# Kernel optimization log

Measured on AMD Instinct MI355X. Metric: run time of the kernel, lower is better.

## Reference

```python
import jax, jax.numpy as jnp
import numpy as np

B, C, N = 4, 256, 4096
C4 = C // 4  # q/k projection dim (channels // 4)
BN_EPS = 1e-5


def setup_inputs() -> dict:
    key = jax.random.key(0)
    ks = jax.random.split(key, 4)
    s = 0.05
    return {
        "x": jax.random.normal(ks[0], (B, C, N), jnp.float32),
        # q_conv and k_conv share this weight in the original module
        "wq": jax.random.normal(ks[1], (C4, C), jnp.float32) * s,
        "wv": jax.random.normal(ks[2], (C, C), jnp.float32) * s,
        "bv": jnp.zeros((C,), jnp.float32),
        "wt": jax.random.normal(ks[3], (C, C), jnp.float32) * s,
        "bt": jnp.zeros((C,), jnp.float32),
        "gamma": jnp.ones((C,), jnp.float32),
        "beta": jnp.zeros((C,), jnp.float32),
        "running_mean": jnp.zeros((C,), jnp.float32),
        "running_var": jnp.ones((C,), jnp.float32),
    }


def reference(x, wq, wv, bv, wt, bt, gamma, beta, running_mean, running_var):
    # 1x1 Conv1d == channel matmul. q/k share wq.
    q = jnp.einsum('oc,bcn->bno', wq, x)            # [B, N, C4]
    k = jnp.einsum('oc,bcn->bon', wq, x)            # [B, C4, N]
    energy = jnp.einsum('bno,bom->bnm', q, k)       # [B, N, N]
    attn = jax.nn.softmax(energy, axis=-1)
    # offset-attention L1 re-normalization over dim 1 (query axis)
    attn = attn / (1e-9 + attn.sum(axis=1, keepdims=True))
    v = jnp.einsum('oc,bcn->bon', wv, x) + bv[None, :, None]   # [B, C, N]
    # x_r[b,c,n] = sum_m v[b,c,m] * attn[b,n,m]
    x_r = jnp.einsum('bcm,bnm->bcn', v, attn)       # [B, C, N]
    t = jnp.einsum('oc,bcn->bon', wt, x - x_r) + bt[None, :, None]
    # BatchNorm1d in inference mode (running stats)
    inv = jax.lax.rsqrt(running_var + BN_EPS)
    bn = (t - running_mean[None, :, None]) * (gamma * inv)[None, :, None] + beta[None, :, None]
    return x + jax.nn.relu(bn)
```

## Files before the change

kernel.cpp:

```cpp
#include <hip/hip_runtime.h>
#include <math.h>

namespace {

constexpr int B_ = 4;
constexpr int C_ = 256;
constexpr int C4_ = 64;
constexpr int N_ = 4096;

typedef __attribute__((ext_vector_type(8))) short bf16x8;
typedef __attribute__((ext_vector_type(4))) float f32x4;
typedef __attribute__((ext_vector_type(16))) float f32x16;

__device__ __forceinline__ unsigned short bf16_rne(float f) {
    unsigned u = __float_as_uint(f);
    u += 0x7fffu + ((u >> 16) & 1u);
    return (unsigned short)(u >> 16);
}

__device__ __forceinline__ void g2l16(const unsigned short* g, unsigned short* l) {
    __builtin_amdgcn_global_load_lds(
        (const __attribute__((address_space(1))) unsigned int*)g,
        (__attribute__((address_space(3))) unsigned int*)l, 16, 0, 0);
}

__global__ __launch_bounds__(256) void cvt_kernel(
        const float* __restrict__ wq, const float* __restrict__ wv,
        const float* __restrict__ wt, unsigned short* __restrict__ wfrag,
        unsigned short* __restrict__ wtb) {
    const int i = (blockIdx.x * 256 + threadIdx.x) * 4;
    const float* src;
    unsigned short* dst;
    if (i < 81920) {
        src = (i < 16384) ? (wq + i) : (wv + (i - 16384));
        const int o = i >> 8, c = i & 255;
        const int gro = o >> 4, l15 = o & 15;
        const int ch = c >> 5, quad = (c >> 3) & 3, e = c & 7;
        dst = wfrag + (((gro * 8 + ch) * 64 + quad * 16 + l15) * 8 + e);
    } else {
        src = wt + (i - 81920);
        dst = wtb + (i - 81920);
    }
    const float4 f = *reinterpret_cast<const float4*>(src);
    ushort4 u;
    u.x = bf16_rne(f.x); u.y = bf16_rne(f.y);
    u.z = bf16_rne(f.z); u.w = bf16_rne(f.w);
    *reinterpret_cast<ushort4*>(dst) = u;
}

__global__ __launch_bounds__(1024, 4) void proj_kernel(
        const float* __restrict__ x, const unsigned short* __restrict__ wfragb,
        const float* __restrict__ bv, unsigned short* __restrict__ qkT,
        unsigned short* __restrict__ v) {
    __shared__ unsigned short xs[2][64][42];
    const int b = blockIdx.y;
    const int n0 = blockIdx.x * 64;
    const int tid = threadIdx.x;
    const int wave = tid >> 6, lane = tid & 63;
    const int ws = wave & 3, oq = wave >> 2;
    const int quad = lane >> 4, l15 = lane & 15;
    const int ca = tid >> 6, na = tid & 63;
    const int cb = (tid + 1024) >> 6, nb2 = (tid + 1024) & 63;
    f32x4 acc[5];
#pragma unroll
    for (int ot = 0; ot < 5; ++ot) acc[ot] = (f32x4){0.f, 0.f, 0.f, 0.f};
    xs[0][na][ca] = bf16_rne(x[((size_t)b * C_ + ca) * N_ + n0 + na]);
    xs[0][nb2][cb] = bf16_rne(x[((size_t)b * C_ + cb) * N_ + n0 + nb2]);
    __syncthreads();
    for (int ch = 0; ch < 8; ++ch) {
        const int buf = ch & 1;
        float la = 0.f, lb = 0.f;
        if (ch < 7) {
            la = x[((size_t)b * C_ + (ch + 1) * 32 + ca) * N_ + n0 + na];
            lb = x[((size_t)b * C_ + (ch + 1) * 32 + cb) * N_ + n0 + nb2];
        }
        const bf16x8 a = *reinterpret_cast<const bf16x8*>(&xs[buf][ws * 16 + l15][quad * 8]);
#pragma unroll
        for (int ot = 0; ot < 5; ++ot) {
            const int gro = oq * 5 + ot;
            const bf16x8 wb = *reinterpret_cast<const bf16x8*>(
                wfragb + (size_t)(((gro * 8 + ch) * 64 + lane) * 8));
            acc[ot] = __builtin_amdgcn_mfma_f32_16x16x32_bf16(a, wb, acc[ot], 0, 0, 0);
        }
        if (ch < 7) {
            xs[buf ^ 1][na][ca] = bf16_rne(la);
            xs[buf ^ 1][nb2][cb] = bf16_rne(lb);
        }
        __syncthreads();
    }
    const int n = n0 + ws * 16 + quad * 4;
#pragma unroll
    for (int ot = 0; ot < 5; ++ot) {
        const int gro = oq * 5 + ot;
        if (gro < 4) {
            const int o = gro * 16 + l15;
#pragma unroll
            for (int r = 0; r < 4; ++r)
                qkT[((size_t)b * N_ + n + r) * C4_ + o] = bf16_rne(acc[ot][r]);
        } else {
            const int c = (gro - 4) * 16 + l15;
            const float bb = bv[c];
            ushort4 u;
            u.x = bf16_rne(acc[ot][0] + bb);
            u.y = bf16_rne(acc[ot][1] + bb);
            u.z = bf16_rne(acc[ot][2] + bb);
            u.w = bf16_rne(acc[ot][3] + bb);
            *reinterpret_cast<ushort4*>(&v[((size_t)b * C_ + c) * N_ + n]) = u;
        }
    }
}

__global__ __launch_bounds__(1024, 4) void rowsum_kernel(
        const unsigned short* __restrict__ qkT, float* __restrict__ rowsuminv) {
    __shared__ unsigned short kt[3][256][64];
    __shared__ float red[2][8][2][16];
    const int gid = blockIdx.x;
    const int xcd = gid & 7;
    const int b = xcd >> 1;
    const int n0 = ((((unsigned)gid >> 3) << 1) | (xcd & 1)) * 64;
    const int tid = threadIdx.x;
    const int wave = tid >> 6, lane = tid & 63;
    const int nt = wave >> 3, ms = wave & 7;
    const int l31 = lane & 31, h = lane >> 5;
    const unsigned short* qb = qkT + (size_t)b * N_ * C4_;
    const int rowA = lane >> 3;
    const int swc = ((lane & 7) ^ rowA) * 8;
    const int w16 = wave * 16;
    const int r7 = l31 & 7;
    const unsigned short* qrow = qb + (size_t)(n0 + nt * 32 + l31) * C4_ + h * 8;
    bf16x8 qa[4];
#pragma unroll
    for (int j = 0; j < 4; ++j)
        qa[j] = *reinterpret_cast<const bf16x8*>(qrow + j * 16);
    asm volatile("s_waitcnt vmcnt(0)" ::: "memory");
#define RS_STAGE(sidx, bufS)                                                  \
    do {                                                                      \
        g2l16(qb + (size_t)((sidx) * 256 + w16 + rowA) * C4_ + swc,           \
              &kt[bufS][w16][0]);                                             \
        g2l16(qb + (size_t)((sidx) * 256 + w16 + 8 + rowA) * C4_ + swc,       \
              &kt[bufS][w16 + 8][0]);                                         \
    } while (0)
    RS_STAGE(0, 0);
    RS_STAGE(1, 1);
    asm volatile("s_waitcnt vmcnt(2)" ::: "memory");
    __builtin_amdgcn_s_barrier();
    f32x16 acc = (f32x16){0.f, 0.f, 0.f, 0.f, 0.f, 0.f, 0.f, 0.f,
                          0.f, 0.f, 0.f, 0.f, 0.f, 0.f, 0.f, 0.f};
    int bufR = 0;
#pragma unroll 1
    for (int t = 0; t < 16; ++t) {
        if (t <= 13) {
            int bufS = bufR + 2; if (bufS >= 3) bufS -= 3;
            RS_STAGE(t + 2, bufS);
        }
        f32x16 z = (f32x16){0.f, 0.f, 0.f, 0.f, 0.f, 0.f, 0.f, 0.f,
                            0.f, 0.f, 0.f, 0.f, 0.f, 0.f, 0.f, 0.f};
        __builtin_amdgcn_s_setprio(1);
#pragma unroll
        for (int j = 0; j < 4; ++j) {
            const bf16x8 kb = *reinterpret_cast<const bf16x8*>(
                &kt[bufR][ms * 32 + l31][(j * 16 + h * 8) ^ (r7 << 3)]);
            z = __builtin_amdgcn_mfma_f32_32x32x16_bf16(qa[j], kb, z, 0, 0, 0);
        }
        __builtin_amdgcn_s_setprio(0);
#pragma unroll
        for (int r = 0; r < 16; ++r) acc[r] += __expf(z[r]);
        asm volatile("s_waitcnt lgkmcnt(0)" ::: "memory");
        if (t <= 13)      asm volatile("s_waitcnt vmcnt(2)" ::: "memory");
        else if (t == 14) asm volatile("s_waitcnt vmcnt(0)" ::: "memory");
        __builtin_amdgcn_s_barrier();
        ++bufR; if (bufR >= 3) bufR = 0;
    }
#undef RS_STAGE
#pragma unroll
    for (int r = 0; r < 16; ++r) {
        float s = acc[r];
#pragma unroll
        for (int k = 1; k <= 16; k <<= 1) s += __shfl_xor(s, k, 64);
        if (l31 == 0) red[nt][ms][h][r] = s;
    }
    __syncthreads();
    if (tid < 64) {
        const int v = tid & 31, nt2 = tid >> 5;
        const int reg = (v & 3) | ((v >> 3) << 2);
        const int hh = (v >> 2) & 1;
        float sum = 0.f;
#pragma unroll
        for (int m = 0; m < 8; ++m) sum += red[nt2][m][hh][reg];
        rowsuminv[(size_t)b * N_ + n0 + nt2 * 32 + v] = 1.0f / sum;
    }
}

__global__ __launch_bounds__(1024, 4) void colsum_kernel(
        const unsigned short* __restrict__ qkT, const float* __restrict__ rowsuminv,
        float* __restrict__ colsuminv) {
    __shared__ float rl[N_];
    __shared__ unsigned short qt[3][256][64];
    __shared__ float red2[8][2][32];
    const int gid = blockIdx.x;
    const int xcd = gid & 7;
    const int b = xcd >> 1;
    const int m0 = ((((unsigned)gid >> 3) << 1) | (xcd & 1)) * 64;
    const int tid = threadIdx.x;
    const int wave = tid >> 6, lane = tid & 63;
    const int ms2 = wave >> 3, ns = wave & 7;
    const int l31 = lane & 31, h = lane >> 5;
    const unsigned short* qb = qkT + (size_t)b * N_ * C4_;
    const int rowA = lane >> 3;
    const int swc = ((lane & 7) ^ rowA) * 8;
    const int w16 = wave * 16;
    const int r7 = l31 & 7;
    for (int i = tid; i < N_; i += 1024) rl[i] = rowsuminv[(size_t)b * N_ + i];
    const unsigned short* krow = qb + (size_t)(m0 + ms2 * 32 + l31) * C4_ + h * 8;
    bf16x8 kbf[4];
#pragma unroll
    for (int j = 0; j < 4; ++j)
        kbf[j] = *reinterpret_cast<const bf16x8*>(krow + j * 16);
    asm volatile("s_waitcnt vmcnt(0)" ::: "memory");
#define CS_STAGE(sidx, bufS)                                                  \
    do {                                                                      \
        g2l16(qb + (size_t)((sidx) * 256 + w16 + rowA) * C4_ + swc,           \
              &qt[bufS][w16][0]);                                             \
        g2l16(qb + (size_t)((sidx) * 256 + w16 + 8 + rowA) * C4_ + swc,       \
              &qt[bufS][w16 + 8][0]);                                         \
    } while (0)
    CS_STAGE(0, 0);
    CS_STAGE(1, 1);
    asm volatile("s_waitcnt vmcnt(2)" ::: "memory");
    asm volatile("s_waitcnt lgkmcnt(0)" ::: "memory");
    __builtin_amdgcn_s_barrier();
    float csa = 0.f;
    int bufR = 0;
#pragma unroll 1
    for (int t = 0; t < 16; ++t) {
        if (t <= 13) {
            int bufS = bufR + 2; if (bufS >= 3) bufS -= 3;
            CS_STAGE(t + 2, bufS);
        }
        f32x16 z = (f32x16){0.f, 0.f, 0.f, 0.f, 0.f, 0.f, 0.f, 0.f,
                            0.f, 0.f, 0.f, 0.f, 0.f, 0.f, 0.f, 0.f};
        __builtin_amdgcn_s_setprio(1);
#pragma unroll
        for (int j = 0; j < 4; ++j) {
            const bf16x8 qa = *reinterpret_cast<const bf16x8*>(
                &qt[bufR][ns * 32 + l31][(j * 16 + h * 8) ^ (r7 << 3)]);
            z = __builtin_amdgcn_mfma_f32_32x32x16_bf16(qa, kbf[j], z, 0, 0, 0);
        }
        __builtin_amdgcn_s_setprio(0);
        const int nb = t * 256 + ns * 32 + 4 * h;
#pragma unroll
        for (int r = 0; r < 16; ++r)
            csa += __expf(z[r]) * rl[nb + (r & 3) + 8 * (r >> 2)];
        asm volatile("s_waitcnt lgkmcnt(0)" ::: "memory");
        if (t <= 13)      asm volatile("s_waitcnt vmcnt(2)" ::: "memory");
        else if (t == 14) asm volatile("s_waitcnt vmcnt(0)" ::: "memory");
        __builtin_amdgcn_s_barrier();
        ++bufR; if (bufR >= 3) bufR = 0;
    }
#undef CS_STAGE
    csa += __shfl_xor(csa, 32, 64);
    if (h == 0) red2[ns][ms2][l31] = csa;
    __syncthreads();
    if (tid < 64) {
        const int ml = tid & 31, mg = tid >> 5;
        float sum = 0.f;
#pragma unroll
        for (int n = 0; n < 8; ++n) sum += red2[n][mg][ml];
        colsuminv[(size_t)b * N_ + m0 + mg * 32 + ml] = 1.0f / (1e-9f + sum);
    }
}

__global__ __launch_bounds__(1024, 4) void final_kernel(
        const float* __restrict__ x, const unsigned short* __restrict__ qkT,
        const unsigned short* __restrict__ v, const unsigned short* __restrict__ wtb,
        const float* __restrict__ rowsuminv, const float* __restrict__ colsuminv,
        const float* __restrict__ bt, const float* __restrict__ gamma,
        const float* __restrict__ beta, const float* __restrict__ rmean,
        const float* __restrict__ rvar, float* __restrict__ out) {
    __shared__ union {
        struct {
            unsigned short vt[3][256][64];
            unsigned short kt[3][64][64];
        } s;
        unsigned short dsm[64][268];
    } u;
    __shared__ unsigned short p_sh[2][4][16][68];
    __shared__ float ci[N_];
    const int gid = blockIdx.x;
    const int xcd = gid & 7;
    const int b = xcd >> 1;
    const int n0 = ((((unsigned)gid >> 3) << 1) | (xcd & 1)) * 64;
    const int tid = threadIdx.x;
    const int wave = tid >> 6, lane = tid & 63;
    const int ws = wave & 3, g = wave >> 2;
    const int quad = lane >> 4, l15 = lane & 15;
    const unsigned short* qb = qkT + (size_t)b * N_ * C4_;
    const unsigned short* vbg = v + (size_t)b * C_ * N_;
    const int rowA = lane >> 3;
    const int swc = ((lane & 7) ^ rowA) * 8;
    const int w8 = wave * 8;
    const int r7 = l15 & 7;
    const int c0s = (quad * 8) ^ (r7 << 3);
    const int c1s = (32 + quad * 8) ^ (r7 << 3);
    const unsigned short* qrow = qb + (size_t)(n0 + ws * 16 + l15) * C4_;
    const bf16x8 q0 = *reinterpret_cast<const bf16x8*>(qrow + quad * 8);
    const bf16x8 q1 = *reinterpret_cast<const bf16x8*>(qrow + 32 + quad * 8);
    const float rli = rowsuminv[(size_t)b * N_ + n0 + ws * 16 + l15];
    {
        const float4 c4 = *reinterpret_cast<const float4*>(colsuminv + (size_t)b * N_ + tid * 4);
        *reinterpret_cast<float4*>(&ci[tid * 4]) = c4;
    }
    asm volatile("s_waitcnt vmcnt(0)" ::: "memory");
#define STAGE_VT(sidx, bufS)                                                            \
    do {                                                                                \
        g2l16(vbg + (size_t)(w8 + rowA) * N_ + (sidx) * 64 + swc,                       \
              &u.s.vt[bufS][w8][0]);                                                    \
        g2l16(vbg + (size_t)(w8 + 128 + rowA) * N_ + (sidx) * 64 + swc,                 \
              &u.s.vt[bufS][w8 + 128][0]);                                              \
    } while (0)
#define STAGE_KT(sidx, bufS)                                                            \
    do {                                                                                \
        if (wave < 8)                                                                   \
            g2l16(qb + (size_t)((sidx) * 64 + w8 + rowA) * C4_ + swc,                   \
                  &u.s.kt[bufS][w8][0]);                                                \
    } while (0)
    STAGE_VT(0, 0);
    STAGE_KT(0, 0);
    STAGE_KT(1, 1);
    asm volatile("s_waitcnt vmcnt(0)" ::: "memory");
    asm volatile("s_waitcnt lgkmcnt(0)" ::: "memory");
    __builtin_amdgcn_s_barrier();
    f32x4 acc[4];
#pragma unroll
    for (int j = 0; j < 4; ++j) acc[j] = (f32x4){0.f, 0.f, 0.f, 0.f};
    int bR = 0;
#pragma unroll 1
    for (int t = 0; t < 64; ++t) {
        int bN = bR + 1; if (bN >= 3) bN -= 3;
        int bN2 = bR + 2; if (bN2 >= 3) bN2 -= 3;
        if (t <= 62) STAGE_VT(t + 1, bN);
        if (t <= 61) STAGE_KT(t + 2, bN2);
        {
            const unsigned short(*ktb)[64] = u.s.kt[bR];
            const bf16x8 ka0 = *reinterpret_cast<const bf16x8*>(&ktb[g * 16 + l15][c0s]);
            const bf16x8 ka1 = *reinterpret_cast<const bf16x8*>(&ktb[g * 16 + l15][c1s]);
            f32x4 z = {0.f, 0.f, 0.f, 0.f};
            z = __builtin_amdgcn_mfma_f32_16x16x32_bf16(ka0, q0, z, 0, 0, 0);
            z = __builtin_amdgcn_mfma_f32_16x16x32_bf16(ka1, q1, z, 0, 0, 0);
            const float4 civ = *reinterpret_cast<const float4*>(&ci[t * 64 + g * 16 + quad * 4]);
            ushort4 pk;
            pk.x = bf16_rne(__expf(z[0]) * rli * civ.x);
            pk.y = bf16_rne(__expf(z[1]) * rli * civ.y);
            pk.z = bf16_rne(__expf(z[2]) * rli * civ.z);
            pk.w = bf16_rne(__expf(z[3]) * rli * civ.w);
            *reinterpret_cast<ushort4*>(&p_sh[t & 1][ws][l15][g * 16 + quad * 4]) = pk;
        }
        if (t) {
            int bP = bR - 1; if (bP < 0) bP += 3;
            const bf16x8 pa0 = *reinterpret_cast<const bf16x8*>(
                &p_sh[(t - 1) & 1][ws][l15][quad * 8]);
            const bf16x8 pa1 = *reinterpret_cast<const bf16x8*>(
                &p_sh[(t - 1) & 1][ws][l15][32 + quad * 8]);
            const unsigned short(*vtb)[64] = u.s.vt[bP];
            __builtin_amdgcn_s_setprio(1);
#pragma unroll
            for (int j = 0; j < 4; ++j) {
                const int vr = (g * 4 + j) * 16 + l15;
                const bf16x8 vb0 = *reinterpret_cast<const bf16x8*>(&vtb[vr][c0s]);
                const bf16x8 vb1 = *reinterpret_cast<const bf16x8*>(&vtb[vr][c1s]);
                acc[j] = __builtin_amdgcn_mfma_f32_16x16x32_bf16(pa0, vb0, acc[j], 0, 0, 0);
                acc[j] = __builtin_amdgcn_mfma_f32_16x16x32_bf16(pa1, vb1, acc[j], 0, 0, 0);
            }
            __builtin_amdgcn_s_setprio(0);
        }
        asm volatile("s_waitcnt lgkmcnt(0)" ::: "memory");
        if (t <= 61) {
            if (wave < 8) asm volatile("s_waitcnt vmcnt(3)" ::: "memory");
            else          asm volatile("s_waitcnt vmcnt(2)" ::: "memory");
        } else if (t == 62) {
            asm volatile("s_waitcnt vmcnt(2)" ::: "memory");
        } else {
            asm volatile("s_waitcnt vmcnt(0)" ::: "memory");
        }
        __builtin_amdgcn_s_barrier();
        ++bR; if (bR >= 3) bR = 0;
    }
    {
        const bf16x8 pa0 = *reinterpret_cast<const bf16x8*>(&p_sh[1][ws][l15][quad * 8]);
        const bf16x8 pa1 = *reinterpret_cast<const bf16x8*>(&p_sh[1][ws][l15][32 + quad * 8]);
        const unsigned short(*vtb)[64] = u.s.vt[0];
#pragma unroll
        for (int j = 0; j < 4; ++j) {
            const int vr = (g * 4 + j) * 16 + l15;
            const bf16x8 vb0 = *reinterpret_cast<const bf16x8*>(&vtb[vr][c0s]);
            const bf16x8 vb1 = *reinterpret_cast<const bf16x8*>(&vtb[vr][c1s]);
            acc[j] = __builtin_amdgcn_mfma_f32_16x16x32_bf16(pa0, vb0, acc[j], 0, 0, 0);
            acc[j] = __builtin_amdgcn_mfma_f32_16x16x32_bf16(pa1, vb1, acc[j], 0, 0, 0);
        }
    }
    __syncthreads();
#pragma unroll
    for (int j = 0; j < 4; ++j) {
        const int c = (g * 4 + j) * 16 + l15;
        const float4 xv = *reinterpret_cast<const float4*>(
            &x[((size_t)b * C_ + c) * N_ + n0 + ws * 16 + quad * 4]);
        const float xvr[4] = {xv.x, xv.y, xv.z, xv.w};
#pragma unroll
        for (int r = 0; r < 4; ++r)
            u.dsm[ws * 16 + quad * 4 + r][c] = bf16_rne(xvr[r] - acc[j][r]);
    }
    __syncthreads();
    bf16x8 da[8];
#pragma unroll
    for (int k = 0; k < 8; ++k)
        da[k] = *reinterpret_cast<const bf16x8*>(&u.dsm[ws * 16 + l15][k * 32 + quad * 8]);
    f32x4 tacc[4];
#pragma unroll
    for (int j = 0; j < 4; ++j) tacc[j] = (f32x4){0.f, 0.f, 0.f, 0.f};
#pragma unroll
    for (int j = 0; j < 4; ++j) {
        const int ot = g * 4 + j;
#pragma unroll
        for (int k = 0; k < 8; ++k) {
            const bf16x8 wb = *reinterpret_cast<const bf16x8*>(
                wtb + (size_t)(ot * 16 + l15) * C_ + k * 32 + quad * 8);
            tacc[j] = __builtin_amdgcn_mfma_f32_16x16x32_bf16(da[k], wb, tacc[j], 0, 0, 0);
        }
    }
#pragma unroll
    for (int j = 0; j < 4; ++j) {
        const int o = (g * 4 + j) * 16 + l15;
        const float gg = gamma[o] * rsqrtf(rvar[o] + 1e-5f);
        const float mn = rmean[o], bbet = beta[o], bo = bt[o];
        const size_t oi = ((size_t)b * C_ + o) * N_ + n0 + ws * 16 + quad * 4;
        const float4 xo = *reinterpret_cast<const float4*>(&x[oi]);
        float4 res;
        res.x = xo.x + fmaxf((tacc[j][0] + bo - mn) * gg + bbet, 0.f);
        res.y = xo.y + fmaxf((tacc[j][1] + bo - mn) * gg + bbet, 0.f);
        res.z = xo.z + fmaxf((tacc[j][2] + bo - mn) * gg + bbet, 0.f);
        res.w = xo.w + fmaxf((tacc[j][3] + bo - mn) * gg + bbet, 0.f);
        *reinterpret_cast<float4*>(&out[oi]) = res;
    }
#undef STAGE_VT
#undef STAGE_KT
}

}

extern "C" void kernel_launch(void* const* d_in, const int* in_sizes, int n_in,
                              void* d_out, int out_size, void* d_ws, size_t ws_size,
                              hipStream_t stream) {
    const float* x = (const float*)d_in[0];
    const float* wq = (const float*)d_in[1];
    const float* wv = (const float*)d_in[2];
    const float* bv = (const float*)d_in[3];
    const float* wt = (const float*)d_in[4];
    const float* bt = (const float*)d_in[5];
    const float* gamma = (const float*)d_in[6];
    const float* beta = (const float*)d_in[7];
    const float* rmean = (const float*)d_in[8];
    const float* rvar = (const float*)d_in[9];
    float* out = (float*)d_out;

    char* base = (char*)d_ws;
    unsigned short* qkT = (unsigned short*)base;
    unsigned short* vw = (unsigned short*)(base + (2u << 20));
    unsigned short* wtb = (unsigned short*)(base + (10u << 20));
    unsigned short* wfrag = (unsigned short*)(base + (10u << 20) + (128u << 10));
    float* rowsuminv = (float*)(base + (10u << 20) + (288u << 10));
    float* colsuminv = (float*)(base + (10u << 20) + (352u << 10));

    cvt_kernel<<<dim3(144), dim3(256), 0, stream>>>(wq, wv, wt, wfrag, wtb);
    proj_kernel<<<dim3(N_ / 64, B_), dim3(1024), 0, stream>>>(x, wfrag, bv, qkT, vw);
    rowsum_kernel<<<dim3(N_ / 64 * B_), dim3(1024), 0, stream>>>(qkT, rowsuminv);
    colsum_kernel<<<dim3(N_ / 64 * B_), dim3(1024), 0, stream>>>(qkT, rowsuminv, colsuminv);
    final_kernel<<<dim3(N_ / 64 * B_), dim3(1024), 0, stream>>>(
        x, qkT, vw, wtb, rowsuminv, colsuminv, bt, gamma, beta, rmean, rvar, out);
}
```

Baseline: 246.6 us.

## Materialize bf16 attention matrix in colsum pass and reuse it in final matmul

When the workspace is large enough, the column-sum kernel writes the row-normalized exp(energy) tile as bf16 into a global N×N buffer per batch. The final kernel then reads that matrix instead of recomputing QK^T and exp. Column normalization is folded into V by a small scaling kernel. This trades recomputing attention for writing and reading about 128 MB of bf16 probabilities through HBM, and adds a rounding step on V.

Result: faster. 223.0 us (-9.6%).

```diff
diff --git a/kernel.cpp b/kernel.cpp
--- a/kernel.cpp
+++ b/kernel.cpp
@@ -16,6 +16,10 @@
     unsigned u = __float_as_uint(f);
     u += 0x7fffu + ((u >> 16) & 1u);
     return (unsigned short)(u >> 16);
+}
+
+__device__ __forceinline__ float bf16_to_f(unsigned short s) {
+    return __uint_as_float(((unsigned)s) << 16);
 }
 
 __device__ __forceinline__ void g2l16(const unsigned short* g, unsigned short* l) {
@@ -191,11 +195,13 @@
     }
 }
 
+template <int WP>
 __global__ __launch_bounds__(1024, 4) void colsum_kernel(
         const unsigned short* __restrict__ qkT, const float* __restrict__ rowsuminv,
-        float* __restrict__ colsuminv) {
+        float* __restrict__ colsuminv, unsigned short* __restrict__ ptg) {
     __shared__ float rl[N_];
     __shared__ unsigned short qt[3][256][64];
+    __shared__ unsigned short ptile[16][32][40];
     __shared__ float red2[8][2][32];
     const int gid = blockIdx.x;
     const int xcd = gid & 7;
@@ -249,11 +255,30 @@
         __builtin_amdgcn_s_setprio(0);
         const int nb = t * 256 + ns * 32 + 4 * h;
 #pragma unroll
-        for (int r = 0; r < 16; ++r)
-            csa += __expf(z[r]) * rl[nb + (r & 3) + 8 * (r >> 2)];
+        for (int r = 0; r < 16; ++r) {
+            const float ex = __expf(z[r]) * rl[nb + (r & 3) + 8 * (r >> 2)];
+            csa += ex;
+            if constexpr (WP)
+                ptile[wave][(r & 3) + 8 * (r >> 2) + 4 * h][l31] = bf16_rne(ex);
+        }
+        if constexpr (WP) {
+            asm volatile("s_waitcnt lgkmcnt(0)" ::: "memory");
+            const int r2 = lane >> 1, hf = lane & 1;
+            const bf16x8 pr0 = *reinterpret_cast<const bf16x8*>(&ptile[wave][r2][hf * 16]);
+            const bf16x8 pr1 = *reinterpret_cast<const bf16x8*>(&ptile[wave][r2][hf * 16 + 8]);
+            unsigned short* pd = ptg + ((size_t)b * N_ + t * 256 + ns * 32 + r2) * N_
+                                 + m0 + ms2 * 32 + hf * 16;
+            *reinterpret_cast<bf16x8*>(pd) = pr0;
+            *reinterpret_cast<bf16x8*>(pd + 8) = pr1;
+        }
         asm volatile("s_waitcnt lgkmcnt(0)" ::: "memory");
-        if (t <= 13)      asm volatile("s_waitcnt vmcnt(2)" ::: "memory");
-        else if (t == 14) asm volatile("s_waitcnt vmcnt(0)" ::: "memory");
+        if constexpr (WP) {
+            if (t <= 13)      asm volatile("s_waitcnt vmcnt(4)" ::: "memory");
+            else if (t == 14) asm volatile("s_waitcnt vmcnt(2)" ::: "memory");
+        } else {
+            if (t <= 13)      asm volatile("s_waitcnt vmcnt(2)" ::: "memory");
+            else if (t == 14) asm volatile("s_waitcnt vmcnt(0)" ::: "memory");
+        }
         __builtin_amdgcn_s_barrier();
         ++bufR; if (bufR >= 3) bufR = 0;
     }
@@ -267,6 +292,152 @@
 #pragma unroll
         for (int n = 0; n < 8; ++n) sum += red2[n][mg][ml];
         colsuminv[(size_t)b * N_ + m0 + mg * 32 + ml] = 1.0f / (1e-9f + sum);
+    }
+}
+
+__global__ __launch_bounds__(256) void scale_v_kernel(
+        unsigned short* __restrict__ v, const float* __restrict__ colsuminv) {
+    const size_t i8 = ((size_t)blockIdx.x * 256 + threadIdx.x) * 8;
+    const int b = (int)(i8 >> 20);
+    const int m = (int)(i8 & 4095);
+    const float* cv = colsuminv + ((size_t)b << 12) + m;
+    const float4 c0 = *reinterpret_cast<const float4*>(cv);
+    const float4 c1 = *reinterpret_cast<const float4*>(cv + 4);
+    const ushort4 a = *reinterpret_cast<const ushort4*>(v + i8);
+    const ushort4 bb = *reinterpret_cast<const ushort4*>(v + i8 + 4);
+    ushort4 oa, ob;
+    oa.x = bf16_rne(bf16_to_f(a.x) * c0.x); oa.y = bf16_rne(bf16_to_f(a.y) * c0.y);
+    oa.z = bf16_rne(bf16_to_f(a.z) * c0.z); oa.w = bf16_rne(bf16_to_f(a.w) * c0.w);
+    ob.x = bf16_rne(bf16_to_f(bb.x) * c1.x); ob.y = bf16_rne(bf16_to_f(bb.y) * c1.y);
+    ob.z = bf16_rne(bf16_to_f(bb.z) * c1.z); ob.w = bf16_rne(bf16_to_f(bb.w) * c1.w);
+    *reinterpret_cast<ushort4*>(v + i8) = oa;
+    *reinterpret_cast<ushort4*>(v + i8 + 4) = ob;
+}
+
+__global__ __launch_bounds__(1024, 4) void final7_kernel(
+        const float* __restrict__ x, const unsigned short* __restrict__ ptg,
+        const unsigned short* __restrict__ v, const unsigned short* __restrict__ wtb,
+        const float* __restrict__ bt, const float* __restrict__ gamma,
+        const float* __restrict__ beta, const float* __restrict__ rmean,
+        const float* __restrict__ rvar, float* __restrict__ out) {
+    __shared__ union {
+        struct {
+            unsigned short vt[3][256][64];
+            unsigned short pt[3][64][64];
+        } s;
+        unsigned short dsm[64][268];
+    } u;
+    const int gid = blockIdx.x;
+    const int xcd = gid & 7;
+    const int b = xcd >> 1;
+    const int n0 = ((((unsigned)gid >> 3) << 1) | (xcd & 1)) * 64;
+    const int tid = threadIdx.x;
+    const int wave = tid >> 6, lane = tid & 63;
+    const int ws = wave & 3, g = wave >> 2;
+    const int quad = lane >> 4, l15 = lane & 15;
+    const unsigned short* pb = ptg + ((size_t)b * N_ + n0) * N_;
+    const unsigned short* vbg = v + (size_t)b * C_ * N_;
+    const int rowA = lane >> 3;
+    const int swc = ((lane & 7) ^ rowA) * 8;
+    const int w8 = wave * 8;
+    const int r7 = l15 & 7;
+    const int c0s = (quad * 8) ^ (r7 << 3);
+    const int c1s = (32 + quad * 8) ^ (r7 << 3);
+    asm volatile("s_waitcnt vmcnt(0)" ::: "memory");
+#define STAGE7(sidx, bufS)                                                              \
+    do {                                                                                \
+        g2l16(vbg + (size_t)(w8 + rowA) * N_ + (sidx) * 64 + swc,                       \
+              &u.s.vt[bufS][w8][0]);                                                    \
+        g2l16(vbg + (size_t)(w8 + 128 + rowA) * N_ + (sidx) * 64 + swc,                 \
+              &u.s.vt[bufS][w8 + 128][0]);                                              \
+        if (wave < 8)                                                                   \
+            g2l16(pb + (size_t)(w8 + rowA) * N_ + (sidx) * 64 + swc,                    \
+                  &u.s.pt[bufS][w8][0]);                                                \
+    } while (0)
+    STAGE7(0, 0);
+    STAGE7(1, 1);
+    if (wave < 8) asm volatile("s_waitcnt vmcnt(3)" ::: "memory");
+    else          asm volatile("s_waitcnt vmcnt(2)" ::: "memory");
+    __builtin_amdgcn_s_barrier();
+    f32x4 acc[4];
+#pragma unroll
+    for (int j = 0; j < 4; ++j) acc[j] = (f32x4){0.f, 0.f, 0.f, 0.f};
+    int bR = 0;
+#pragma unroll 1
+    for (int t = 0; t < 64; ++t) {
+        if (t <= 61) {
+            int bN2 = bR + 2; if (bN2 >= 3) bN2 -= 3;
+            STAGE7(t + 2, bN2);
+        }
+        {
+            const bf16x8 pa0 = *reinterpret_cast<const bf16x8*>(
+                &u.s.pt[bR][ws * 16 + l15][c0s]);
+            const bf16x8 pa1 = *reinterpret_cast<const bf16x8*>(
+                &u.s.pt[bR][ws * 16 + l15][c1s]);
+            const unsigned short(*vtb)[64] = u.s.vt[bR];
+            __builtin_amdgcn_s_setprio(1);
+#pragma unroll
+            for (int j = 0; j < 4; ++j) {
+                const int vr = (g * 4 + j) * 16 + l15;
+                const bf16x8 vb0 = *reinterpret_cast<const bf16x8*>(&vtb[vr][c0s]);
+                const bf16x8 vb1 = *reinterpret_cast<const bf16x8*>(&vtb[vr][c1s]);
+                acc[j] = __builtin_amdgcn_mfma_f32_16x16x32_bf16(pa0, vb0, acc[j], 0, 0, 0);
+                acc[j] = __builtin_amdgcn_mfma_f32_16x16x32_bf16(pa1, vb1, acc[j], 0, 0, 0);
+            }
+            __builtin_amdgcn_s_setprio(0);
+        }
+        asm volatile("s_waitcnt lgkmcnt(0)" ::: "memory");
+        if (t <= 61) {
+            if (wave < 8) asm volatile("s_waitcnt vmcnt(3)" ::: "memory");
+            else          asm volatile("s_waitcnt vmcnt(2)" ::: "memory");
+        } else if (t == 62) {
+            asm volatile("s_waitcnt vmcnt(0)" ::: "memory");
+        }
+        __builtin_amdgcn_s_barrier();
+        ++bR; if (bR >= 3) bR = 0;
+    }
+#undef STAGE7
+#pragma unroll
+    for (int j = 0; j < 4; ++j) {
+        const int c = (g * 4 + j) * 16 + l15;
+        const float4 xv = *reinterpret_cast<const float4*>(
+            &x[((size_t)b * C_ + c) * N_ + n0 + ws * 16 + quad * 4]);
+        const float xvr[4] = {xv.x, xv.y, xv.z, xv.w};
+#pragma unroll
+        for (int r = 0; r < 4; ++r)
+            u.dsm[ws * 16 + quad * 4 + r][c] = bf16_rne(xvr[r] - acc[j][r]);
+    }
+    __syncthreads();
+    bf16x8 da[8];
+#pragma unroll
+    for (int k = 0; k < 8; ++k)
+        da[k] = *reinterpret_cast<const bf16x8*>(&u.dsm[ws * 16 + l15][k * 32 + quad * 8]);
+    f32x4 tacc[4];
+#pragma unroll
+    for (int j = 0; j < 4; ++j) tacc[j] = (f32x4){0.f, 0.f, 0.f, 0.f};
+#pragma unroll
+    for (int j = 0; j < 4; ++j) {
+        const int ot = g * 4 + j;
+#pragma unroll
+        for (int k = 0; k < 8; ++k) {
+            const bf16x8 wb = *reinterpret_cast<const bf16x8*>(
+                wtb + (size_t)(ot * 16 + l15) * C_ + k * 32 + quad * 8);
+            tacc[j] = __builtin_amdgcn_mfma_f32_16x16x32_bf16(da[k], wb, tacc[j], 0, 0, 0);
+        }
+    }
+#pragma unroll
+    for (int j = 0; j < 4; ++j) {
+        const int o = (g * 4 + j) * 16 + l15;
+        const float gg = gamma[o] * rsqrtf(rvar[o] + 1e-5f);
+        const float mn = rmean[o], bbet = beta[o], bo = bt[o];
+        const size_t oi = ((size_t)b * C_ + o) * N_ + n0 + ws * 16 + quad * 4;
+        const float4 xo = *reinterpret_cast<const float4*>(&x[oi]);
+        float4 res;
+        res.x = xo.x + fmaxf((tacc[j][0] + bo - mn) * gg + bbet, 0.f);
+        res.y = xo.y + fmaxf((tacc[j][1] + bo - mn) * gg + bbet, 0.f);
+        res.z = xo.z + fmaxf((tacc[j][2] + bo - mn) * gg + bbet, 0.f);
+        res.w = xo.w + fmaxf((tacc[j][3] + bo - mn) * gg + bbet, 0.f);
+        *reinterpret_cast<float4*>(&out[oi]) = res;
     }
 }
 
@@ -469,11 +640,22 @@
     unsigned short* wfrag = (unsigned short*)(base + (10u << 20) + (128u << 10));
     float* rowsuminv = (float*)(base + (10u << 20) + (288u << 10));
     float* colsuminv = (float*)(base + (10u << 20) + (352u << 10));
+    unsigned short* ptg = (unsigned short*)(base + (16ull << 20));
+    const bool big = ws_size >= (144ull << 20);
 
     cvt_kernel<<<dim3(144), dim3(256), 0, stream>>>(wq, wv, wt, wfrag, wtb);
     proj_kernel<<<dim3(N_ / 64, B_), dim3(1024), 0, stream>>>(x, wfrag, bv, qkT, vw);
     rowsum_kernel<<<dim3(N_ / 64 * B_), dim3(1024), 0, stream>>>(qkT, rowsuminv);
-    colsum_kernel<<<dim3(N_ / 64 * B_), dim3(1024), 0, stream>>>(qkT, rowsuminv, colsuminv);
-    final_kernel<<<dim3(N_ / 64 * B_), dim3(1024), 0, stream>>>(
-        x, qkT, vw, wtb, rowsuminv, colsuminv, bt, gamma, beta, rmean, rvar, out);
-}
+    if (big) {
+        colsum_kernel<1><<<dim3(N_ / 64 * B_), dim3(1024), 0, stream>>>(
+            qkT, rowsuminv, colsuminv, ptg);
+        scale_v_kernel<<<dim3(2048), dim3(256), 0, stream>>>(vw, colsuminv);
+        final7_kernel<<<dim3(N_ / 64 * B_), dim3(1024), 0, stream>>>(
+            x, ptg, vw, wtb, bt, gamma, beta, rmean, rvar, out);
+    } else {
+        colsum_kernel<0><<<dim3(N_ / 64 * B_), dim3(1024), 0, stream>>>(
+            qkT, rowsuminv, colsuminv, nullptr);
+        final_kernel<<<dim3(N_ / 64 * B_), dim3(1024), 0, stream>>>(
+            x, qkT, vw, wtb, rowsuminv, colsuminv, bt, gamma, beta, rmean, rvar, out);
+    }
+}
```

## Materialize exp(QK^T) once in bf16 and reuse it for colsum and final

Applied to the files above, without the earlier changes.

The rowsum kernel now writes the full exp(energy) matrix in bf16 to global workspace, about 128 MB. It also computes weighted partial column sums, which replaces the separate colsum kernel that recomputed QK^T and exp. The column normalisation is folded into V through a new scale kernel, and the row normalisation is applied in the epilogue of the final kernel. The final kernel streams the stored P tiles instead of recomputing them with MFMA and exp. This trades recomputation for a very large HBM write and read of the attention matrix, and adds two small kernels.

After: 226.0 us. 1.09x faster.

```diff
diff --git a/kernel.cpp b/kernel.cpp
--- a/kernel.cpp
+++ b/kernel.cpp
@@ -16,6 +16,10 @@
     unsigned u = __float_as_uint(f);
     u += 0x7fffu + ((u >> 16) & 1u);
     return (unsigned short)(u >> 16);
+}
+
+__device__ __forceinline__ float bf16_to_f(unsigned short s) {
+    return __uint_as_float(((unsigned)s) << 16);
 }
 
 __device__ __forceinline__ void g2l16(const unsigned short* g, unsigned short* l) {
@@ -111,9 +115,12 @@
 }
 
 __global__ __launch_bounds__(1024, 4) void rowsum_kernel(
-        const unsigned short* __restrict__ qkT, float* __restrict__ rowsuminv) {
+        const unsigned short* __restrict__ qkT, float* __restrict__ rowsuminv,
+        unsigned short* __restrict__ etg, float* __restrict__ psum) {
     __shared__ unsigned short kt[3][256][64];
+    __shared__ unsigned short etile[16][32][40];
     __shared__ float red[2][8][2][16];
+    __shared__ float rls[64];
     const int gid = blockIdx.x;
     const int xcd = gid & 7;
     const int b = xcd >> 1;
@@ -164,14 +171,29 @@
         }
         __builtin_amdgcn_s_setprio(0);
 #pragma unroll
-        for (int r = 0; r < 16; ++r) acc[r] += __expf(z[r]);
+        for (int r = 0; r < 16; ++r) {
+            const float ex = __expf(z[r]);
+            acc[r] += ex;
+            etile[wave][(r & 3) + 8 * (r >> 2) + 4 * h][l31] = bf16_rne(ex);
+        }
         asm volatile("s_waitcnt lgkmcnt(0)" ::: "memory");
-        if (t <= 13)      asm volatile("s_waitcnt vmcnt(2)" ::: "memory");
-        else if (t == 14) asm volatile("s_waitcnt vmcnt(0)" ::: "memory");
+        {
+            const int r2 = lane >> 1, hf = lane & 1;
+            const bf16x8 pr0 = *reinterpret_cast<const bf16x8*>(&etile[wave][r2][hf * 16]);
+            const bf16x8 pr1 = *reinterpret_cast<const bf16x8*>(&etile[wave][r2][hf * 16 + 8]);
+            unsigned short* pd = etg + ((size_t)b * N_ + n0 + nt * 32 + r2) * N_
+                                 + t * 256 + ms * 32 + hf * 16;
+            *reinterpret_cast<bf16x8*>(pd) = pr0;
+            *reinterpret_cast<bf16x8*>(pd + 8) = pr1;
+        }
+        asm volatile("s_waitcnt lgkmcnt(0)" ::: "memory");
+        if (t <= 13)      asm volatile("s_waitcnt vmcnt(4)" ::: "memory");
+        else if (t == 14) asm volatile("s_waitcnt vmcnt(2)" ::: "memory");
         __builtin_amdgcn_s_barrier();
         ++bufR; if (bufR >= 3) bufR = 0;
     }
 #undef RS_STAGE
+    asm volatile("s_waitcnt vmcnt(0)" ::: "memory");
 #pragma unroll
     for (int r = 0; r < 16; ++r) {
         float s = acc[r];
@@ -187,105 +209,71 @@
         float sum = 0.f;
 #pragma unroll
         for (int m = 0; m < 8; ++m) sum += red[nt2][m][hh][reg];
-        rowsuminv[(size_t)b * N_ + n0 + nt2 * 32 + v] = 1.0f / sum;
-    }
-}
-
-__global__ __launch_bounds__(1024, 4) void colsum_kernel(
-        const unsigned short* __restrict__ qkT, const float* __restrict__ rowsuminv,
-        float* __restrict__ colsuminv) {
-    __shared__ float rl[N_];
-    __shared__ unsigned short qt[3][256][64];
-    __shared__ float red2[8][2][32];
-    const int gid = blockIdx.x;
-    const int xcd = gid & 7;
-    const int b = xcd >> 1;
-    const int m0 = ((((unsigned)gid >> 3) << 1) | (xcd & 1)) * 64;
-    const int tid = threadIdx.x;
-    const int wave = tid >> 6, lane = tid & 63;
-    const int ms2 = wave >> 3, ns = wave & 7;
-    const int l31 = lane & 31, h = lane >> 5;
-    const unsigned short* qb = qkT + (size_t)b * N_ * C4_;
-    const int rowA = lane >> 3;
-    const int swc = ((lane & 7) ^ rowA) * 8;
-    const int w16 = wave * 16;
-    const int r7 = l31 & 7;
-    for (int i = tid; i < N_; i += 1024) rl[i] = rowsuminv[(size_t)b * N_ + i];
-    const unsigned short* krow = qb + (size_t)(m0 + ms2 * 32 + l31) * C4_ + h * 8;
-    bf16x8 kbf[4];
-#pragma unroll
-    for (int j = 0; j < 4; ++j)
-        kbf[j] = *reinterpret_cast<const bf16x8*>(krow + j * 16);
-    asm volatile("s_waitcnt vmcnt(0)" ::: "memory");
-#define CS_STAGE(sidx, bufS)                                                  \
-    do {                                                                      \
-        g2l16(qb + (size_t)((sidx) * 256 + w16 + rowA) * C4_ + swc,           \
-              &qt[bufS][w16][0]);                                             \
-        g2l16(qb + (size_t)((sidx) * 256 + w16 + 8 + rowA) * C4_ + swc,       \
-              &qt[bufS][w16 + 8][0]);                                         \
-    } while (0)
-    CS_STAGE(0, 0);
-    CS_STAGE(1, 1);
-    asm volatile("s_waitcnt vmcnt(2)" ::: "memory");
-    asm volatile("s_waitcnt lgkmcnt(0)" ::: "memory");
-    __builtin_amdgcn_s_barrier();
-    float csa = 0.f;
-    int bufR = 0;
-#pragma unroll 1
-    for (int t = 0; t < 16; ++t) {
-        if (t <= 13) {
-            int bufS = bufR + 2; if (bufS >= 3) bufS -= 3;
-            CS_STAGE(t + 2, bufS);
-        }
-        f32x16 z = (f32x16){0.f, 0.f, 0.f, 0.f, 0.f, 0.f, 0.f, 0.f,
-                            0.f, 0.f, 0.f, 0.f, 0.f, 0.f, 0.f, 0.f};
-        __builtin_amdgcn_s_setprio(1);
-#pragma unroll
-        for (int j = 0; j < 4; ++j) {
-            const bf16x8 qa = *reinterpret_cast<const bf16x8*>(
-                &qt[bufR][ns * 32 + l31][(j * 16 + h * 8) ^ (r7 << 3)]);
-            z = __builtin_amdgcn_mfma_f32_32x32x16_bf16(qa, kbf[j], z, 0, 0, 0);
-        }
-        __builtin_amdgcn_s_setprio(0);
-        const int nb = t * 256 + ns * 32 + 4 * h;
-#pragma unroll
-        for (int r = 0; r < 16; ++r)
-            csa += __expf(z[r]) * rl[nb + (r & 3) + 8 * (r >> 2)];
-        asm volatile("s_waitcnt lgkmcnt(0)" ::: "memory");
-        if (t <= 13)      asm volatile("s_waitcnt vmcnt(2)" ::: "memory");
-        else if (t == 14) asm volatile("s_waitcnt vmcnt(0)" ::: "memory");
-        __builtin_amdgcn_s_barrier();
-        ++bufR; if (bufR >= 3) bufR = 0;
-    }
-#undef CS_STAGE
-    csa += __shfl_xor(csa, 32, 64);
-    if (h == 0) red2[ns][ms2][l31] = csa;
+        const float inv = 1.0f / sum;
+        rowsuminv[(size_t)b * N_ + n0 + nt2 * 32 + v] = inv;
+        rls[nt2 * 32 + v] = inv;
+    }
     __syncthreads();
-    if (tid < 64) {
-        const int ml = tid & 31, mg = tid >> 5;
-        float sum = 0.f;
-#pragma unroll
-        for (int n = 0; n < 8; ++n) sum += red2[n][mg][ml];
-        colsuminv[(size_t)b * N_ + m0 + mg * 32 + ml] = 1.0f / (1e-9f + sum);
-    }
-}
-
-__global__ __launch_bounds__(1024, 4) void final_kernel(
-        const float* __restrict__ x, const unsigned short* __restrict__ qkT,
+    float p0 = 0.f, p1 = 0.f, p2 = 0.f, p3 = 0.f;
+    const unsigned short* eb = etg + ((size_t)b * N_ + n0) * N_ + tid * 4;
+#pragma unroll 4
+    for (int nn = 0; nn < 64; ++nn) {
+        const float w = rls[nn];
+        const ushort4 ev = *reinterpret_cast<const ushort4*>(eb + (size_t)nn * N_);
+        p0 += bf16_to_f(ev.x) * w;
+        p1 += bf16_to_f(ev.y) * w;
+        p2 += bf16_to_f(ev.z) * w;
+        p3 += bf16_to_f(ev.w) * w;
+    }
+    const float4 st = {p0, p1, p2, p3};
+    *reinterpret_cast<float4*>(
+        psum + ((size_t)b * 64 + (n0 >> 6)) * (size_t)N_ + tid * 4) = st;
+}
+
+__global__ __launch_bounds__(256) void civ_kernel(
+        const float* __restrict__ psum, float* __restrict__ colsuminv) {
+    const int idx = blockIdx.x * 256 + threadIdx.x;
+    const int b = idx >> 12, m = idx & 4095;
+    const float* p = psum + (size_t)b * 64 * N_ + m;
+    float s = 0.f;
+#pragma unroll 8
+    for (int k = 0; k < 64; ++k) s += p[(size_t)k * N_];
+    colsuminv[(size_t)b * N_ + m] = 1.0f / (1e-9f + s);
+}
+
+__global__ __launch_bounds__(256) void scale_v_kernel(
+        unsigned short* __restrict__ v, const float* __restrict__ colsuminv) {
+    const size_t i8 = ((size_t)blockIdx.x * 256 + threadIdx.x) * 8;
+    const int b = (int)(i8 >> 20);
+    const int m = (int)(i8 & 4095);
+    const float* cv = colsuminv + ((size_t)b << 12) + m;
+    const float4 c0 = *reinterpret_cast<const float4*>(cv);
+    const float4 c1 = *reinterpret_cast<const float4*>(cv + 4);
+    const ushort4 a = *reinterpret_cast<const ushort4*>(v + i8);
+    const ushort4 bb = *reinterpret_cast<const ushort4*>(v + i8 + 4);
+    ushort4 oa, ob;
+    oa.x = bf16_rne(bf16_to_f(a.x) * c0.x); oa.y = bf16_rne(bf16_to_f(a.y) * c0.y);
+    oa.z = bf16_rne(bf16_to_f(a.z) * c0.z); oa.w = bf16_rne(bf16_to_f(a.w) * c0.w);
+    ob.x = bf16_rne(bf16_to_f(bb.x) * c1.x); ob.y = bf16_rne(bf16_to_f(bb.y) * c1.y);
+    ob.z = bf16_rne(bf16_to_f(bb.z) * c1.z); ob.w = bf16_rne(bf16_to_f(bb.w) * c1.w);
+    *reinterpret_cast<ushort4*>(v + i8) = oa;
+    *reinterpret_cast<ushort4*>(v + i8 + 4) = ob;
+}
+
+__global__ __launch_bounds__(1024, 4) void final7_kernel(
+        const float* __restrict__ x, const unsigned short* __restrict__ etg,
         const unsigned short* __restrict__ v, const unsigned short* __restrict__ wtb,
-        const float* __restrict__ rowsuminv, const float* __restrict__ colsuminv,
-        const float* __restrict__ bt, const float* __restrict__ gamma,
-        const float* __restrict__ beta, const float* __restrict__ rmean,
-        const float* __restrict__ rvar, float* __restrict__ out) {
+        const float* __restrict__ rowsuminv, const float* __restrict__ bt,
+        const float* __restrict__ gamma, const float* __restrict__ beta,
+        const float* __restrict__ rmean, const float* __restrict__ rvar,
+        float* __restrict__ out) {
     __shared__ union {
         struct {
             unsigned short vt[3][256][64];
-            unsigned short kt[3][64][64];
+            unsigned short pt[3][64][64];
         } s;
         unsigned short dsm[64][268];
     } u;
-    __shared__ unsigned short p_sh[2][4][16][68];
-    __shared__ float ci[N_];
     const int gid = blockIdx.x;
     const int xcd = gid & 7;
     const int b = xcd >> 1;
@@ -294,7 +282,7 @@
     const int wave = tid >> 6, lane = tid & 63;
     const int ws = wave & 3, g = wave >> 2;
     const int quad = lane >> 4, l15 = lane & 15;
-    const unsigned short* qb = qkT + (size_t)b * N_ * C4_;
+    const unsigned short* pb = etg + ((size_t)b * N_ + n0) * N_;
     const unsigned short* vbg = v + (size_t)b * C_ * N_;
     const int rowA = lane >> 3;
     const int swc = ((lane & 7) ^ rowA) * 8;
@@ -302,33 +290,24 @@
     const int r7 = l15 & 7;
     const int c0s = (quad * 8) ^ (r7 << 3);
     const int c1s = (32 + quad * 8) ^ (r7 << 3);
-    const unsigned short* qrow = qb + (size_t)(n0 + ws * 16 + l15) * C4_;
-    const bf16x8 q0 = *reinterpret_cast<const bf16x8*>(qrow + quad * 8);
-    const bf16x8 q1 = *reinterpret_cast<const bf16x8*>(qrow + 32 + quad * 8);
-    const float rli = rowsuminv[(size_t)b * N_ + n0 + ws * 16 + l15];
-    {
-        const float4 c4 = *reinterpret_cast<const float4*>(colsuminv + (size_t)b * N_ + tid * 4);
-        *reinterpret_cast<float4*>(&ci[tid * 4]) = c4;
-    }
+    const float4 rlv = *reinterpret_cast<const float4*>(
+        rowsuminv + (size_t)b * N_ + n0 + ws * 16 + quad * 4);
+    const float rlr[4] = {rlv.x, rlv.y, rlv.z, rlv.w};
     asm volatile("s_waitcnt vmcnt(0)" ::: "memory");
-#define STAGE_VT(sidx, bufS)                                                            \
+#define STAGE7(sidx, bufS)                                                              \
     do {                                                                                \
         g2l16(vbg + (size_t)(w8 + rowA) * N_ + (sidx) * 64 + swc,                       \
               &u.s.vt[bufS][w8][0]);                                                    \
         g2l16(vbg + (size_t)(w8 + 128 + rowA) * N_ + (sidx) * 64 + swc,                 \
               &u.s.vt[bufS][w8 + 128][0]);                                              \
+        if (wave < 8)                                                                   \
+            g2l16(pb + (size_t)(w8 + rowA) * N_ + (sidx) * 64 + swc,                    \
+                  &u.s.pt[bufS][w8][0]);                                                \
     } while (0)
-#define STAGE_KT(sidx, bufS)                                                            \
-    do {                                                                                \
-        if (wave < 8)                                                                   \
-            g2l16(qb + (size_t)((sidx) * 64 + w8 + rowA) * C4_ + swc,                   \
-                  &u.s.kt[bufS][w8][0]);                                                \
-    } while (0)
-    STAGE_VT(0, 0);
-    STAGE_KT(0, 0);
-    STAGE_KT(1, 1);
-    asm volatile("s_waitcnt vmcnt(0)" ::: "memory");
-    asm volatile("s_waitcnt lgkmcnt(0)" ::: "memory");
+    STAGE7(0, 0);
+    STAGE7(1, 1);
+    if (wave < 8) asm volatile("s_waitcnt vmcnt(3)" ::: "memory");
+    else          asm volatile("s_waitcnt vmcnt(2)" ::: "memory");
     __builtin_amdgcn_s_barrier();
     f32x4 acc[4];
 #pragma unroll
@@ -336,32 +315,16 @@
     int bR = 0;
 #pragma unroll 1
     for (int t = 0; t < 64; ++t) {
-        int bN = bR + 1; if (bN >= 3) bN -= 3;
-        int bN2 = bR + 2; if (bN2 >= 3) bN2 -= 3;
-        if (t <= 62) STAGE_VT(t + 1, bN);
-        if (t <= 61) STAGE_KT(t + 2, bN2);
+        if (t <= 61) {
+            int bN2 = bR + 2; if (bN2 >= 3) bN2 -= 3;
+            STAGE7(t + 2, bN2);
+        }
         {
-            const unsigned short(*ktb)[64] = u.s.kt[bR];
-            const bf16x8 ka0 = *reinterpret_cast<const bf16x8*>(&ktb[g * 16 + l15][c0s]);
-            const bf16x8 ka1 = *reinterpret_cast<const bf16x8*>(&ktb[g * 16 + l15][c1s]);
-            f32x4 z = {0.f, 0.f, 0.f, 0.f};
-            z = __builtin_amdgcn_mfma_f32_16x16x32_bf16(ka0, q0, z, 0, 0, 0);
-            z = __builtin_amdgcn_mfma_f32_16x16x32_bf16(ka1, q1, z, 0, 0, 0);
-            const float4 civ = *reinterpret_cast<const float4*>(&ci[t * 64 + g * 16 + quad * 4]);
-            ushort4 pk;
-            pk.x = bf16_rne(__expf(z[0]) * rli * civ.x);
-            pk.y = bf16_rne(__expf(z[1]) * rli * civ.y);
-            pk.z = bf16_rne(__expf(z[2]) * rli * civ.z);
-            pk.w = bf16_rne(__expf(z[3]) * rli * civ.w);
-            *reinterpret_cast<ushort4*>(&p_sh[t & 1][ws][l15][g * 16 + quad * 4]) = pk;
-        }
-        if (t) {
-            int bP = bR - 1; if (bP < 0) bP += 3;
             const bf16x8 pa0 = *reinterpret_cast<const bf16x8*>(
-                &p_sh[(t - 1) & 1][ws][l15][quad * 8]);
+                &u.s.pt[bR][ws * 16 + l15][c0s]);
             const bf16x8 pa1 = *reinterpret_cast<const bf16x8*>(
-                &p_sh[(t - 1) & 1][ws][l15][32 + quad * 8]);
-            const unsigned short(*vtb)[64] = u.s.vt[bP];
+                &u.s.pt[bR][ws * 16 + l15][c1s]);
+            const unsigned short(*vtb)[64] = u.s.vt[bR];
             __builtin_amdgcn_s_setprio(1);
 #pragma unroll
             for (int j = 0; j < 4; ++j) {
@@ -378,27 +341,12 @@
             if (wave < 8) asm volatile("s_waitcnt vmcnt(3)" ::: "memory");
             else          asm volatile("s_waitcnt vmcnt(2)" ::: "memory");
         } else if (t == 62) {
-            asm volatile("s_waitcnt vmcnt(2)" ::: "memory");
-        } else {
             asm volatile("s_waitcnt vmcnt(0)" ::: "memory");
         }
         __builtin_amdgcn_s_barrier();
         ++bR; if (bR >= 3) bR = 0;
     }
-    {
-        const bf16x8 pa0 = *reinterpret_cast<const bf16x8*>(&p_sh[1][ws][l15][quad * 8]);
-        const bf16x8 pa1 = *reinterpret_cast<const bf16x8*>(&p_sh[1][ws][l15][32 + quad * 8]);
-        const unsigned short(*vtb)[64] = u.s.vt[0];
-#pragma unroll
-        for (int j = 0; j < 4; ++j) {
-            const int vr = (g * 4 + j) * 16 + l15;
-            const bf16x8 vb0 = *reinterpret_cast<const bf16x8*>(&vtb[vr][c0s]);
-            const bf16x8 vb1 = *reinterpret_cast<const bf16x8*>(&vtb[vr][c1s]);
-            acc[j] = __builtin_amdgcn_mfma_f32_16x16x32_bf16(pa0, vb0, acc[j], 0, 0, 0);
-            acc[j] = __builtin_amdgcn_mfma_f32_16x16x32_bf16(pa1, vb1, acc[j], 0, 0, 0);
-        }
-    }
-    __syncthreads();
+#undef STAGE7
 #pragma unroll
     for (int j = 0; j < 4; ++j) {
         const int c = (g * 4 + j) * 16 + l15;
@@ -407,7 +355,7 @@
         const float xvr[4] = {xv.x, xv.y, xv.z, xv.w};
 #pragma unroll
         for (int r = 0; r < 4; ++r)
-            u.dsm[ws * 16 + quad * 4 + r][c] = bf16_rne(xvr[r] - acc[j][r]);
+            u.dsm[ws * 16 + quad * 4 + r][c] = bf16_rne(xvr[r] - acc[j][r] * rlr[r]);
     }
     __syncthreads();
     bf16x8 da[8];
@@ -441,8 +389,6 @@
         res.w = xo.w + fmaxf((tacc[j][3] + bo - mn) * gg + bbet, 0.f);
         *reinterpret_cast<float4*>(&out[oi]) = res;
     }
-#undef STAGE_VT
-#undef STAGE_KT
 }
 
 }
@@ -469,11 +415,15 @@
     unsigned short* wfrag = (unsigned short*)(base + (10u << 20) + (128u << 10));
     float* rowsuminv = (float*)(base + (10u << 20) + (288u << 10));
     float* colsuminv = (float*)(base + (10u << 20) + (352u << 10));
+    float* psum = (float*)(base + (11u << 20));
+    unsigned short* etg = (unsigned short*)(base + (16ull << 20));
 
     cvt_kernel<<<dim3(144), dim3(256), 0, stream>>>(wq, wv, wt, wfrag, wtb);
     proj_kernel<<<dim3(N_ / 64, B_), dim3(1024), 0, stream>>>(x, wfrag, bv, qkT, vw);
-    rowsum_kernel<<<dim3(N_ / 64 * B_), dim3(1024), 0, stream>>>(qkT, rowsuminv);
-    colsum_kernel<<<dim3(N_ / 64 * B_), dim3(1024), 0, stream>>>(qkT, rowsuminv, colsuminv);
-    final_kernel<<<dim3(N_ / 64 * B_), dim3(1024), 0, stream>>>(
-        x, qkT, vw, wtb, rowsuminv, colsuminv, bt, gamma, beta, rmean, rvar, out);
-}
+    rowsum_kernel<<<dim3(N_ / 64 * B_), dim3(1024), 0, stream>>>(
+        qkT, rowsuminv, etg, psum);
+    civ_kernel<<<dim3(64), dim3(256), 0, stream>>>(psum, colsuminv);
+    scale_v_kernel<<<dim3(2048), dim3(256), 0, stream>>>(vw, colsuminv);
+    final7_kernel<<<dim3(N_ / 64 * B_), dim3(1024), 0, stream>>>(
+        x, etg, vw, wtb, rowsuminv, bt, gamma, beta, rmean, rvar, out);
+}
```
